# Kernel optimization log

Measured on AMD Instinct MI355X. Metric: run time of the kernel, lower is better.

The kernel has to match this reference:

```python
import jax, jax.numpy as jnp
from jax import lax
import numpy as np

N_FEATURES, HIDDEN, LATENT = 51, 64, 24
BATCH, SEQ = 2048, 100


def _lstm_params(key, in_dim, hid):
    k = 1.0 / np.sqrt(hid)
    ks = jax.random.split(key, 4)
    u = lambda kk, shape: jax.random.uniform(kk, shape, jnp.float32, -k, k)
    return (u(ks[0], (4 * hid, in_dim)),  # W_ih, torch gate order i,f,g,o
            u(ks[1], (4 * hid, hid)),     # W_hh
            u(ks[2], (4 * hid,)),         # b_ih
            u(ks[3], (4 * hid,)))         # b_hh


def lstm(x, w_ih, w_hh, b_ih, b_hh):
    """Batch-first single-layer LSTM matching torch.nn.LSTM (zero init state).
    x: [B,T,I] -> (outputs [B,T,H], final hidden [B,H])."""
    B = x.shape[0]
    H = w_hh.shape[1]
    # Precompute the input contribution for all timesteps in one GEMM.
    xg = jnp.einsum('bti,gi->btg', x, w_ih) + b_ih + b_hh  # [B,T,4H]

    def step(carry, xt):
        h, c = carry
        g = xt + h @ w_hh.T                       # [B,4H]
        i, f, gg, o = jnp.split(g, 4, axis=-1)    # torch order i,f,g,o
        i = jax.nn.sigmoid(i)
        f = jax.nn.sigmoid(f)
        gg = jnp.tanh(gg)
        o = jax.nn.sigmoid(o)
        c = f * c + i * gg
        h = o * jnp.tanh(c)
        return (h, c), h

    init = (jnp.zeros((B, H), x.dtype), jnp.zeros((B, H), x.dtype))
    (h_n, _), ys = lax.scan(step, init, jnp.swapaxes(xg, 0, 1))
    return jnp.swapaxes(ys, 0, 1), h_n


def setup_inputs() -> dict:
    key = jax.random.key(0)
    ks = jax.random.split(key, 6)
    x = jax.random.normal(ks[0], (BATCH, SEQ, N_FEATURES), jnp.float32)
    e1 = _lstm_params(ks[1], N_FEATURES, HIDDEN)
    e2 = _lstm_params(ks[2], HIDDEN, LATENT)
    d1 = _lstm_params(ks[3], LATENT, HIDDEN)
    d2 = _lstm_params(ks[4], HIDDEN, HIDDEN)
    kw, kb = jax.random.split(ks[5])
    kk = 1.0 / np.sqrt(HIDDEN)
    w_out = jax.random.uniform(kw, (N_FEATURES, HIDDEN), jnp.float32, -kk, kk)
    b_out = jax.random.uniform(kb, (N_FEATURES,), jnp.float32, -kk, kk)
    return {
        'x': x,
        'e1_wih': e1[0], 'e1_whh': e1[1], 'e1_bih': e1[2], 'e1_bhh': e1[3],
        'e2_wih': e2[0], 'e2_whh': e2[1], 'e2_bih': e2[2], 'e2_bhh': e2[3],
        'd1_wih': d1[0], 'd1_whh': d1[1], 'd1_bih': d1[2], 'd1_bhh': d1[3],
        'd2_wih': d2[0], 'd2_whh': d2[1], 'd2_bih': d2[2], 'd2_bhh': d2[3],
        'w_out': w_out, 'b_out': b_out,
    }


def reference(x,
              e1_wih, e1_whh, e1_bih, e1_bhh,
              e2_wih, e2_whh, e2_bih, e2_bhh,
              d1_wih, d1_whh, d1_bih, d1_bhh,
              d2_wih, d2_whh, d2_bih, d2_bhh,
              w_out, b_out):
    seq_len = x.shape[1]
    # Encode (dropout is identity at inference, p=0.1 train-only)
    out1, _ = lstm(x, e1_wih, e1_whh, e1_bih, e1_bhh)          # [B,T,hidden]
    _, z = lstm(out1, e2_wih, e2_whh, e2_bih, e2_bhh)          # hn -> [B,latent]
    # Decode: repeat latent across time
    rep = jnp.broadcast_to(z[:, None, :], (z.shape[0], seq_len, z.shape[1]))
    d_out1, _ = lstm(rep, d1_wih, d1_whh, d1_bih, d1_bhh)      # [B,T,hidden]
    d_out2, _ = lstm(d_out1, d2_wih, d2_whh, d2_bih, d2_bhh)   # [B,T,hidden]
    recon = jnp.einsum('bth,fh->btf', d_out2, w_out) + b_out   # [B,T,n_features]
    return recon
```

## Files before the change

kernel.cpp:

```cpp
#include <hip/hip_runtime.h>
#include <stdint.h>

typedef __attribute__((ext_vector_type(8))) __bf16 bf16x8;
typedef __attribute__((ext_vector_type(4))) float f32x4;
typedef __attribute__((ext_vector_type(4))) unsigned int uint4v;

#define DI __device__ __forceinline__
#define MFMA_(a,b,c) __builtin_amdgcn_mfma_f32_16x16x32_bf16(a,b,c,0,0,0)

static constexpr int B_ = 2048;
static constexpr int T_ = 100;

DI float bf2f(unsigned short u){
  unsigned int i = ((unsigned int)u) << 16;
  float f; __builtin_memcpy(&f, &i, 4); return f;
}
DI unsigned short f2bf(float f){
  unsigned int x; __builtin_memcpy(&x, &f, 4);
  unsigned int r = (x + 0x7fffu + ((x >> 16) & 1u)) >> 16;
  return (unsigned short)r;
}
DI unsigned int pk2bf(float a, float b){
  unsigned int r;
  asm("v_cvt_pk_bf16_f32 %0, %1, %2" : "=v"(r) : "v"(a), "v"(b));
  return r;
}
DI float rcp_(float x){ return __builtin_amdgcn_rcpf(x); }
DI float sig_(float x){ return rcp_(1.0f + __expf(-x)); }
DI float tanh_(float x){ return 1.0f - 2.0f * rcp_(__expf(2.0f * x) + 1.0f); }

template<int KS>
DI f32x4 dot1(const bf16x8* a, const bf16x8* b, f32x4 acc)
{
  #pragma unroll
  for (int s = 0; s < KS; ++s)
    acc = MFMA_(a[s], b[s], acc);
  return acc;
}

DI void pw(const f32x4 (&acc)[4], float (&cc)[4], float (&hv)[4],
           unsigned short (&hH)[4])
{
  #pragma unroll
  for (int r = 0; r < 4; ++r){
    float iv = sig_(acc[0][r]);
    float fv = sig_(acc[1][r]);
    float gv = tanh_(acc[2][r]);
    float ov = sig_(acc[3][r]);
    cc[r] = fv * cc[r] + iv * gv;
    hv[r] = ov * tanh_(cc[r]);
  }
  unsigned int u01 = pk2bf(hv[0], hv[1]);
  unsigned int u23 = pk2bf(hv[2], hv[3]);
  hH[0] = (unsigned short)u01; hH[1] = (unsigned short)(u01 >> 16);
  hH[2] = (unsigned short)u23; hH[3] = (unsigned short)(u23 >> 16);
}

__global__ __launch_bounds__(256) void prep_frags(
    const float* __restrict__ e1_wih, const float* __restrict__ e1_whh,
    const float* __restrict__ e2_wih, const float* __restrict__ e2_whh,
    const float* __restrict__ d1_whh,
    const float* __restrict__ d2_wih, const float* __restrict__ d2_whh,
    const float* __restrict__ w_out,
    unsigned short* __restrict__ dst)
{
  int fid = blockIdx.x * 256 + threadIdx.x;
  if (fid >= 12288) return;
  int layer, local, KS;
  if (fid < 4096)      { layer = 0; local = fid;         KS = 4; }
  else if (fid < 5632) { layer = 1; local = fid - 4096;  KS = 3; }
  else if (fid < 7680) { layer = 2; local = fid - 5632;  KS = 2; }
  else if (fid < 11776){ layer = 3; local = fid - 7680;  KS = 4; }
  else                 { layer = 4; local = fid - 11776; KS = 2; }
  int lane = local & 63;
  int ns = local >> 6;
  int s = ns % KS, n = ns / KS;
  int col = 16 * n + (lane & 15);
  int kb = 32 * s + 8 * (lane >> 4);
  union { unsigned short u[8]; uint4v v; } pk;
  #pragma unroll
  for (int e = 0; e < 8; ++e){
    int k = kb + e;
    float w = 0.0f;
    if (layer == 0){
      if (k < 51) w = e1_wih[col * 51 + k];
      else if (k >= 64) w = e1_whh[col * 64 + (k - 64)];
    } else if (layer == 1){
      int q = col >> 5, jj = col & 31;
      if (jj < 24){
        int r = q * 24 + jj;
        if (k < 64) w = e2_wih[r * 64 + k];
        else if (k < 88) w = e2_whh[r * 24 + (k - 64)];
      }
    } else if (layer == 2){
      w = d1_whh[col * 64 + k];
    } else if (layer == 3){
      if (k < 64) w = d2_wih[col * 64 + k];
      else w = d2_whh[col * 64 + (k - 64)];
    } else {
      if (col < 51) w = w_out[col * 64 + k];
    }
    pk.u[e] = f2bf(w);
  }
  *(uint4v*)(dst + (size_t)fid * 8) = pk.v;
}

__global__ __launch_bounds__(256) void gx_k(
    const float* __restrict__ z, const float* __restrict__ d1_wih,
    const float* __restrict__ bih, const float* __restrict__ bhh,
    float* __restrict__ gx)
{
  int s = blockIdx.x, col = threadIdx.x;
  float acc = bih[col] + bhh[col];
  #pragma unroll
  for (int k = 0; k < 24; ++k)
    acc += z[s * 24 + k] * d1_wih[col * 24 + k];
  gx[s * 256 + col] = acc;
}

__global__ __launch_bounds__(512, 1) void fused_enc(
    const float* xseq,
    const unsigned short* __restrict__ bf1u,
    const unsigned short* __restrict__ bf2u,
    const float* __restrict__ e1_bih, const float* __restrict__ e1_bhh,
    const float* __restrict__ e2_bih, const float* __restrict__ e2_bhh,
    float* __restrict__ zout)
{
  constexpr int SA1 = 136;
  constexpr int SB2 = 40;
  __shared__ __align__(16) unsigned short A1H[2][16 * SA1];
  __shared__ __align__(16) unsigned short A2B[2][16 * SB2];

  const int tid = threadIdx.x, wid = tid >> 6, lane = tid & 63;
  const int l15 = lane & 15, l4 = lane >> 4;
  const size_t s0 = (size_t)blockIdx.x * 16;
  const bool isE1 = (wid < 4);
  const bool isE2 = (wid == 4 || wid == 5);
  const bool isXW = (wid >= 6);
  const int jj1 = 16 * wid + l15;
  const int jj2 = 16 * (wid - 4) + l15;
  const int xt = tid - 384;

  const bf16x8* f1 = (const bf16x8*)bf1u;
  const bf16x8* f2 = (const bf16x8*)bf2u;
  bf16x8 b1H[16];
  f32x4 init1[4];
  if (isE1){
    #pragma unroll
    for (int g = 0; g < 4; ++g){
      #pragma unroll
      for (int s = 0; s < 4; ++s)
        b1H[g * 4 + s] = f1[(size_t)(((wid + 4 * g) * 4 + s) * 64 + lane)];
      float b = e1_bih[g * 64 + jj1] + e1_bhh[g * 64 + jj1];
      init1[g] = (f32x4){b, b, b, b};
    }
  }
  bf16x8 b2H[12];
  f32x4 init2[4];
  if (isE2){
    #pragma unroll
    for (int g = 0; g < 4; ++g){
      #pragma unroll
      for (int s = 0; s < 3; ++s)
        b2H[g * 3 + s] = f2[(size_t)((((wid - 4) + 2 * g) * 3 + s) * 64 + lane)];
      float b2 = (jj2 < 24) ? (e2_bih[g * 24 + jj2] + e2_bhh[g * 24 + jj2]) : 0.0f;
      init2[g] = (f32x4){b2, b2, b2, b2};
    }
  }

  for (int i = tid; i < 16 * SA1; i += 512){ A1H[0][i] = 0; A1H[1][i] = 0; }
  for (int i = tid; i < 16 * SB2; i += 512){ A2B[0][i] = 0; A2B[1][i] = 0; }
  __syncthreads();
  #pragma unroll
  for (int it = 0; it < 2; ++it){
    int idx = tid + it * 512, row = idx >> 6, k = idx & 63;
    float v = (k < 51) ? xseq[((s0 + row) * T_ + 0) * 51 + k] : 0.0f;
    A1H[0][row * SA1 + k] = f2bf(v);
  }
  __syncthreads();

  float xsA[8], xsB[8];
  if (isXW){
    #pragma unroll
    for (int it = 0; it < 8; ++it){
      int idx = xt + it * 128, row = idx >> 6, k = idx & 63;
      xsA[it] = (k < 51) ? xseq[((s0 + row) * T_ + 1) * 51 + k] : 0.0f;
      xsB[it] = (k < 51) ? xseq[((s0 + row) * T_ + 2) * 51 + k] : 0.0f;
    }
  }
  float cc1[4] = {0.f,0.f,0.f,0.f}, cc2[4] = {0.f,0.f,0.f,0.f};

#define ENC_STEP(TCUR, BSEL, XW)                                               \
  {                                                                            \
    const int t = (TCUR);                                                      \
    if (isE1 && t < T_){                                        \
      bf16x8 a1H[4];                                                           \
      _Pragma("unroll")                                                        \
      for (int s = 0; s < 4; ++s)                                              \
        a1H[s] = *(const bf16x8*)&A1H[BSEL][l15 * SA1 + 32 * s + 8 * l4];      \
      f32x4 acc[4];                                                            \
      _Pragma("unroll")                                                        \
      for (int g = 0; g < 4; ++g)                                              \
        acc[g] = dot1<4>(a1H, &b1H[g * 4], init1[g]);                          \
      float hv[4]; unsigned short hH[4];                                       \
      pw(acc, cc1, hv, hH);                                                    \
      _Pragma("unroll")                                                        \
      for (int r = 0; r < 4; ++r)                                              \
        A1H[BSEL ^ 1][(4 * l4 + r) * SA1 + 64 + jj1] = hH[r];                  \
    }                                                                          \
    if (isE2 && t >= 1 && t <= T_){                  \
      bf16x8 af2[3];                                                           \
      af2[0] = *(const bf16x8*)&A1H[BSEL][l15 * SA1 + 64 + 8 * l4];            \
      af2[1] = *(const bf16x8*)&A1H[BSEL][l15 * SA1 + 96 + 8 * l4];            \
      af2[2] = *(const bf16x8*)&A2B[BSEL][l15 * SB2 + 8 * l4];                 \
      f32x4 acc[4];                                                            \
      _Pragma("unroll")                                                        \
      for (int g = 0; g < 4; ++g)                                              \
        acc[g] = dot1<3>(af2, &b2H[g * 3], init2[g]);                          \
      float hv[4]; unsigned short hH[4];                                       \
      pw(acc, cc2, hv, hH);                                                    \
      if (jj2 < 24){                                                           \
        _Pragma("unroll")                                                      \
        for (int r = 0; r < 4; ++r)                                            \
          A2B[BSEL ^ 1][(4 * l4 + r) * SB2 + jj2] = hH[r];                     \
        if (t == T_){                                                          \
          _Pragma("unroll")                                                    \
          for (int r = 0; r < 4; ++r)                                          \
            zout[(s0 + 4 * l4 + r) * 24 + jj2] = hv[r];                        \
        }                                                                      \
      }                                                                        \
    }                                                                          \
    if (isXW && t + 1 < T_){             \
      _Pragma("unroll")                                                        \
      for (int it = 0; it < 8; it += 2){                                       \
        int idx = xt + it * 128;                                               \
        int row0_ = idx >> 6, k0_ = idx & 63;                                  \
        int row1_ = (idx + 128) >> 6, k1_ = (idx + 128) & 63;                  \
        unsigned int u = pk2bf(XW[it], XW[it + 1]);                            \
        A1H[BSEL ^ 1][row0_ * SA1 + k0_] = (unsigned short)u;                  \
        A1H[BSEL ^ 1][row1_ * SA1 + k1_] = (unsigned short)(u >> 16);          \
      }                                                                        \
      if (t + 3 < T_){                                                         \
        _Pragma("unroll")                                                      \
        for (int it = 0; it < 8; ++it){                                        \
          int idx = xt + it * 128, row = idx >> 6, k = idx & 63;               \
          XW[it] = (k < 51) ? xseq[((s0 + row) * T_ + (t + 3)) * 51 + k] : 0.0f; \
        }                                                                      \
      }                                                                        \
    }                                                                          \
    asm volatile("s_waitcnt lgkmcnt(0)\n\ts_barrier" ::: "memory");            \
  }

  #pragma unroll 1
  for (int tt = 0; tt < 102; tt += 2){
    ENC_STEP(tt,     0, xsA)
    ENC_STEP(tt + 1, 1, xsB)
  }
#undef ENC_STEP
}

__global__ __launch_bounds__(512, 1) void fused_dec(
    const float* __restrict__ gxin,
    const unsigned short* __restrict__ bf3u,
    const unsigned short* __restrict__ bf4u,
    const unsigned short* __restrict__ bfpu,
    const float* __restrict__ d2_bih, const float* __restrict__ d2_bhh,
    const float* __restrict__ b_out,
    float* out)
{
  constexpr int SA4 = 136;
  __shared__ __align__(16) unsigned short A4H[2][16 * SA4];

  const int tid = threadIdx.x, wid = tid >> 6, lane = tid & 63;
  const int l15 = lane & 15, l4 = lane >> 4;
  const size_t s0 = (size_t)blockIdx.x * 16;
  const bool isD1 = (wid < 4);
  const int jj3 = 16 * wid + l15;
  const int jj4 = 16 * (wid - 4) + l15;

  const bf16x8* f3 = (const bf16x8*)bf3u;
  const bf16x8* f4 = (const bf16x8*)bf4u;
  const bf16x8* fp = (const bf16x8*)bfpu;
  bf16x8 b3H[8], bpH[2];
  f32x4 init3[4], biasP;
  if (isD1){
    #pragma unroll
    for (int g = 0; g < 4; ++g){
      #pragma unroll
      for (int s = 0; s < 2; ++s)
        b3H[g * 2 + s] = f3[(size_t)(((wid + 4 * g) * 2 + s) * 64 + lane)];
      #pragma unroll
      for (int r = 0; r < 4; ++r)
        init3[g][r] = gxin[(s0 + 4 * l4 + r) * 256 + jj3 + 64 * g];
    }
    #pragma unroll
    for (int s = 0; s < 2; ++s)
      bpH[s] = fp[(size_t)((wid * 2 + s) * 64 + lane)];
    float bp = (jj3 < 51) ? b_out[jj3] : 0.0f;
    biasP = (f32x4){bp, bp, bp, bp};
  }
  bf16x8 b4H[16];
  f32x4 init4[4];
  if (!isD1){
    #pragma unroll
    for (int g = 0; g < 4; ++g){
      #pragma unroll
      for (int s = 0; s < 4; ++s)
        b4H[g * 4 + s] = f4[(size_t)((((wid - 4) + 4 * g) * 4 + s) * 64 + lane)];
      float b = d2_bih[g * 64 + jj4] + d2_bhh[g * 64 + jj4];
      init4[g] = (f32x4){b, b, b, b};
    }
  }

  for (int i = tid; i < 16 * SA4; i += 512){ A4H[0][i] = 0; A4H[1][i] = 0; }
  __syncthreads();

  float cc3[4] = {0.f,0.f,0.f,0.f}, cc4[4] = {0.f,0.f,0.f,0.f};

#define DEC_STEP(TCUR, BSEL)                                                   \
  {                                                                            \
    const int t = (TCUR);                                                      \
    bf16x8 a4[4];                                                              \
    _Pragma("unroll")                                                          \
    for (int s = 0; s < 4; ++s)                                                \
      a4[s] = *(const bf16x8*)&A4H[BSEL][l15 * SA4 + 32 * s + 8 * l4];         \
    if (isD1){                                                                 \
      if (t < T_){                     \
        f32x4 acc[4];                                                          \
        _Pragma("unroll")                                                      \
        for (int g = 0; g < 4; ++g)                                            \
          acc[g] = dot1<2>(a4, &b3H[g * 2], init3[g]);                         \
        float hv[4]; unsigned short hH[4];                                     \
        pw(acc, cc3, hv, hH);                                                  \
        _Pragma("unroll")                                                      \
        for (int r = 0; r < 4; ++r)                                            \
          A4H[BSEL ^ 1][(4 * l4 + r) * SA4 + jj3] = hH[r];                     \
      }                                                                        \
      if (t >= 2){                          \
        f32x4 pr = dot1<2>(&a4[2], bpH, biasP);                                \
        if (jj3 < 51){                                                         \
          _Pragma("unroll")                                                    \
          for (int r = 0; r < 4; ++r)                                          \
            out[((s0 + 4 * l4 + r) * T_ + (t - 2)) * 51 + jj3] = pr[r];        \
        }                                                                      \
      }                                                                        \
    } else {                                                                   \
      if (t >= 1 && t <= T_){                        \
        f32x4 acc[4];                                                          \
        _Pragma("unroll")                                                      \
        for (int g = 0; g < 4; ++g)                                            \
          acc[g] = dot1<4>(a4, &b4H[g * 4], init4[g]);                         \
        float hv[4]; unsigned short hH[4];                                     \
        pw(acc, cc4, hv, hH);                                                  \
        _Pragma("unroll")                                                      \
        for (int r = 0; r < 4; ++r)                                            \
          A4H[BSEL ^ 1][(4 * l4 + r) * SA4 + 64 + jj4] = hH[r];                \
      }                                                                        \
    }                                                                          \
    asm volatile("s_waitcnt lgkmcnt(0)\n\ts_barrier" ::: "memory");            \
  }

  #pragma unroll 1
  for (int tt = 0; tt < 102; tt += 2){
    DEC_STEP(tt,     0)
    DEC_STEP(tt + 1, 1)
  }
#undef DEC_STEP
}

extern "C" void kernel_launch(void* const* d_in, const int* in_sizes, int n_in,
                              void* d_out, int out_size, void* d_ws, size_t ws_size,
                              hipStream_t stream)
{
  (void)in_sizes; (void)n_in; (void)out_size; (void)ws_size;
  const float* x      = (const float*)d_in[0];
  const float* e1_wih = (const float*)d_in[1];
  const float* e1_whh = (const float*)d_in[2];
  const float* e1_bih = (const float*)d_in[3];
  const float* e1_bhh = (const float*)d_in[4];
  const float* e2_wih = (const float*)d_in[5];
  const float* e2_whh = (const float*)d_in[6];
  const float* e2_bih = (const float*)d_in[7];
  const float* e2_bhh = (const float*)d_in[8];
  const float* d1_wih = (const float*)d_in[9];
  const float* d1_whh = (const float*)d_in[10];
  const float* d1_bih = (const float*)d_in[11];
  const float* d1_bhh = (const float*)d_in[12];
  const float* d2_wih = (const float*)d_in[13];
  const float* d2_whh = (const float*)d_in[14];
  const float* d2_bih = (const float*)d_in[15];
  const float* d2_bhh = (const float*)d_in[16];
  const float* w_out  = (const float*)d_in[17];
  const float* b_out  = (const float*)d_in[18];

  char* ws = (char*)d_ws;
  unsigned short* bfrag = (unsigned short*)ws;
  const size_t OF_L2 = 4096 * 8, OF_L3 = 5632 * 8, OF_L4 = 7680 * 8, OF_PR = 11776 * 8;
  float* zbuf  = (float*)(ws + 196608);
  float* gxbuf = (float*)(ws + 196608 + 196608);

  prep_frags<<<48, 256, 0, stream>>>(e1_wih, e1_whh, e2_wih, e2_whh,
                                     d1_whh, d2_wih, d2_whh, w_out, bfrag);
  fused_enc<<<128, 512, 0, stream>>>(
      x, bfrag, bfrag + OF_L2, e1_bih, e1_bhh, e2_bih, e2_bhh, zbuf);
  gx_k<<<2048, 256, 0, stream>>>(zbuf, d1_wih, d1_bih, d1_bhh, gxbuf);
  fused_dec<<<128, 512, 0, stream>>>(
      gxbuf, bfrag + OF_L3, bfrag + OF_L4, bfrag + OF_PR,
      d2_bih, d2_bhh, b_out, (float*)d_out);
}
```

Baseline: 172.6 us.

## Fuse encoder, latent projection and decoder into one persistent kernel

Merges the encoder kernel, the small gx projection kernel and the decoder kernel into a single kernel. The latent z stays in shared memory and the d1 input projection is computed in registers, so the z and gx buffers no longer go through global memory. The time loops are peeled into prologue, steady-state and epilogue steps, which removes per-step bounds checks and lets shared-memory loads be issued before the MFMA work. This saves two kernel launches and a global round trip, at the cost of higher register pressure in one large kernel.

```diff
diff --git a/kernel.cpp b/kernel.cpp
--- a/kernel.cpp
+++ b/kernel.cpp
@@ -105,99 +105,97 @@
   *(uint4v*)(dst + (size_t)fid * 8) = pk.v;
 }
 
-__global__ __launch_bounds__(256) void gx_k(
-    const float* __restrict__ z, const float* __restrict__ d1_wih,
-    const float* __restrict__ bih, const float* __restrict__ bhh,
-    float* __restrict__ gx)
-{
-  int s = blockIdx.x, col = threadIdx.x;
-  float acc = bih[col] + bhh[col];
-  #pragma unroll
-  for (int k = 0; k < 24; ++k)
-    acc += z[s * 24 + k] * d1_wih[col * 24 + k];
-  gx[s * 256 + col] = acc;
-}
-
-__global__ __launch_bounds__(512, 1) void fused_enc(
+__global__ __launch_bounds__(512, 1) void fused_all(
     const float* xseq,
-    const unsigned short* __restrict__ bf1u,
-    const unsigned short* __restrict__ bf2u,
+    const unsigned short* __restrict__ bfr,
     const float* __restrict__ e1_bih, const float* __restrict__ e1_bhh,
     const float* __restrict__ e2_bih, const float* __restrict__ e2_bhh,
-    float* __restrict__ zout)
+    const float* __restrict__ d1_wih, const float* __restrict__ d1_bih,
+    const float* __restrict__ d1_bhh,
+    const float* __restrict__ d2_bih, const float* __restrict__ d2_bhh,
+    const float* __restrict__ b_out,
+    float* out)
 {
-  constexpr int SA1 = 136;
+  constexpr int SA = 136;
   constexpr int SB2 = 40;
-  __shared__ __align__(16) unsigned short A1H[2][16 * SA1];
+  constexpr size_t OF_L2 = 4096, OF_L3 = 5632, OF_L4 = 7680, OF_PR = 11776;
+  __shared__ __align__(16) unsigned short AST[2][16 * SA];
   __shared__ __align__(16) unsigned short A2B[2][16 * SB2];
+  __shared__ float zS[16][24];
 
   const int tid = threadIdx.x, wid = tid >> 6, lane = tid & 63;
   const int l15 = lane & 15, l4 = lane >> 4;
   const size_t s0 = (size_t)blockIdx.x * 16;
-  const bool isE1 = (wid < 4);
-  const bool isE2 = (wid == 4 || wid == 5);
-  const bool isXW = (wid >= 6);
-  const int jj1 = 16 * wid + l15;
-  const int jj2 = 16 * (wid - 4) + l15;
-  const int xt = tid - 384;
-
-  const bf16x8* f1 = (const bf16x8*)bf1u;
-  const bf16x8* f2 = (const bf16x8*)bf2u;
-  bf16x8 b1H[16];
-  f32x4 init1[4];
-  if (isE1){
+  const bf16x8* fr = (const bf16x8*)bfr;
+
+  {
+    const bool isE1 = (wid < 4);
+    const bool isE2 = (wid == 4 || wid == 5);
+    const bool isXW = (wid >= 6);
+    const int jj1 = 16 * wid + l15;
+    const int jj2 = 16 * (wid - 4) + l15;
+    const int xt = tid - 384;
+
+    bf16x8 b1H[16]; f32x4 init1[4];
+    if (isE1){
+      #pragma unroll
+      for (int g = 0; g < 4; ++g){
+        #pragma unroll
+        for (int s = 0; s < 4; ++s)
+          b1H[g * 4 + s] = fr[(size_t)(((wid + 4 * g) * 4 + s) * 64 + lane)];
+        float b = e1_bih[g * 64 + jj1] + e1_bhh[g * 64 + jj1];
+        init1[g] = (f32x4){b, b, b, b};
+      }
+    }
+    bf16x8 b2H[12]; f32x4 init2[4];
+    if (isE2){
+      #pragma unroll
+      for (int g = 0; g < 4; ++g){
+        #pragma unroll
+        for (int s = 0; s < 3; ++s)
+          b2H[g * 3 + s] = fr[OF_L2 + (size_t)((((wid - 4) + 2 * g) * 3 + s) * 64 + lane)];
+        float b2 = (jj2 < 24) ? (e2_bih[g * 24 + jj2] + e2_bhh[g * 24 + jj2]) : 0.0f;
+        init2[g] = (f32x4){b2, b2, b2, b2};
+      }
+    }
+
+    for (int i = tid; i < 16 * SA; i += 512){ AST[0][i] = 0; AST[1][i] = 0; }
+    for (int i = tid; i < 16 * SB2; i += 512){ A2B[0][i] = 0; A2B[1][i] = 0; }
+    __syncthreads();
     #pragma unroll
-    for (int g = 0; g < 4; ++g){
-      #pragma unroll
-      for (int s = 0; s < 4; ++s)
-        b1H[g * 4 + s] = f1[(size_t)(((wid + 4 * g) * 4 + s) * 64 + lane)];
-      float b = e1_bih[g * 64 + jj1] + e1_bhh[g * 64 + jj1];
-      init1[g] = (f32x4){b, b, b, b};
-    }
-  }
-  bf16x8 b2H[12];
-  f32x4 init2[4];
-  if (isE2){
-    #pragma unroll
-    for (int g = 0; g < 4; ++g){
-      #pragma unroll
-      for (int s = 0; s < 3; ++s)
-        b2H[g * 3 + s] = f2[(size_t)((((wid - 4) + 2 * g) * 3 + s) * 64 + lane)];
-      float b2 = (jj2 < 24) ? (e2_bih[g * 24 + jj2] + e2_bhh[g * 24 + jj2]) : 0.0f;
-      init2[g] = (f32x4){b2, b2, b2, b2};
-    }
-  }
-
-  for (int i = tid; i < 16 * SA1; i += 512){ A1H[0][i] = 0; A1H[1][i] = 0; }
-  for (int i = tid; i < 16 * SB2; i += 512){ A2B[0][i] = 0; A2B[1][i] = 0; }
-  __syncthreads();
-  #pragma unroll
-  for (int it = 0; it < 2; ++it){
-    int idx = tid + it * 512, row = idx >> 6, k = idx & 63;
-    float v = (k < 51) ? xseq[((s0 + row) * T_ + 0) * 51 + k] : 0.0f;
-    A1H[0][row * SA1 + k] = f2bf(v);
-  }
-  __syncthreads();
-
-  float xsA[8], xsB[8];
-  if (isXW){
-    #pragma unroll
-    for (int it = 0; it < 8; ++it){
-      int idx = xt + it * 128, row = idx >> 6, k = idx & 63;
-      xsA[it] = (k < 51) ? xseq[((s0 + row) * T_ + 1) * 51 + k] : 0.0f;
-      xsB[it] = (k < 51) ? xseq[((s0 + row) * T_ + 2) * 51 + k] : 0.0f;
-    }
-  }
-  float cc1[4] = {0.f,0.f,0.f,0.f}, cc2[4] = {0.f,0.f,0.f,0.f};
-
-#define ENC_STEP(TCUR, BSEL, XW)                                               \
+    for (int it = 0; it < 2; ++it){
+      int idx = tid + it * 512, row = idx >> 6, k = idx & 63;
+      float v = (k < 51) ? xseq[((s0 + row) * T_ + 0) * 51 + k] : 0.0f;
+      AST[0][row * SA + k] = f2bf(v);
+    }
+    __syncthreads();
+
+    float xsA[8], xsB[8];
+    if (isXW){
+      #pragma unroll
+      for (int it = 0; it < 8; ++it){
+        int idx = xt + it * 128, row = idx >> 6, k = idx & 63;
+        xsA[it] = (k < 51) ? xseq[((s0 + row) * T_ + 1) * 51 + k] : 0.0f;
+        xsB[it] = (k < 51) ? xseq[((s0 + row) * T_ + 2) * 51 + k] : 0.0f;
+      }
+    }
+    float cc1[4] = {0.f,0.f,0.f,0.f}, cc2[4] = {0.f,0.f,0.f,0.f};
+
+#define E_STEP(TT, BS, XW, D1, D2, DZ)                                         \
   {                                                                            \
-    const int t = (TCUR);                                                      \
-    if (isE1 && t < T_){                                        \
-      bf16x8 a1H[4];                                                           \
+    const int t = (TT);                                                        \
+    bf16x8 a1H[4]; bf16x8 af2[3];                                              \
+    if ((D1) && isE1){                                                         \
       _Pragma("unroll")                                                        \
       for (int s = 0; s < 4; ++s)                                              \
-        a1H[s] = *(const bf16x8*)&A1H[BSEL][l15 * SA1 + 32 * s + 8 * l4];      \
+        a1H[s] = *(const bf16x8*)&AST[BS][l15 * SA + 32 * s + 8 * l4];         \
+    }                                                                          \
+    if ((D2) && isE2){                                                         \
+      af2[0] = *(const bf16x8*)&AST[BS][l15 * SA + 64 + 8 * l4];               \
+      af2[1] = *(const bf16x8*)&AST[BS][l15 * SA + 96 + 8 * l4];               \
+      af2[2] = *(const bf16x8*)&A2B[BS][l15 * SB2 + 8 * l4];                   \
+    }                                                                          \
+    if ((D1) && isE1){                                                         \
       f32x4 acc[4];                                                            \
       _Pragma("unroll")                                                        \
       for (int g = 0; g < 4; ++g)                                              \
@@ -206,39 +204,17 @@
       pw(acc, cc1, hv, hH);                                                    \
       _Pragma("unroll")                                                        \
       for (int r = 0; r < 4; ++r)                                              \
-        A1H[BSEL ^ 1][(4 * l4 + r) * SA1 + 64 + jj1] = hH[r];                  \
-    }                                                                          \
-    if (isE2 && t >= 1 && t <= T_){                  \
-      bf16x8 af2[3];                                                           \
-      af2[0] = *(const bf16x8*)&A1H[BSEL][l15 * SA1 + 64 + 8 * l4];            \
-      af2[1] = *(const bf16x8*)&A1H[BSEL][l15 * SA1 + 96 + 8 * l4];            \
-      af2[2] = *(const bf16x8*)&A2B[BSEL][l15 * SB2 + 8 * l4];                 \
-      f32x4 acc[4];                                                            \
-      _Pragma("unroll")                                                        \
-      for (int g = 0; g < 4; ++g)                                              \
-        acc[g] = dot1<3>(af2, &b2H[g * 3], init2[g]);                          \
-      float hv[4]; unsigned short hH[4];                                       \
-      pw(acc, cc2, hv, hH);                                                    \
-      if (jj2 < 24){                                                           \
-        _Pragma("unroll")                                                      \
-        for (int r = 0; r < 4; ++r)                                            \
-          A2B[BSEL ^ 1][(4 * l4 + r) * SB2 + jj2] = hH[r];                     \
-        if (t == T_){                                                          \
-          _Pragma("unroll")                                                    \
-          for (int r = 0; r < 4; ++r)                                          \
-            zout[(s0 + 4 * l4 + r) * 24 + jj2] = hv[r];                        \
-        }                                                                      \
-      }                                                                        \
-    }                                                                          \
-    if (isXW && t + 1 < T_){             \
+        AST[BS ^ 1][(4 * l4 + r) * SA + 64 + jj1] = hH[r];                     \
+    }                                                                          \
+    if ((D1) && isXW && t + 1 < T_){                                           \
       _Pragma("unroll")                                                        \
       for (int it = 0; it < 8; it += 2){                                       \
         int idx = xt + it * 128;                                               \
         int row0_ = idx >> 6, k0_ = idx & 63;                                  \
         int row1_ = (idx + 128) >> 6, k1_ = (idx + 128) & 63;                  \
         unsigned int u = pk2bf(XW[it], XW[it + 1]);                            \
-        A1H[BSEL ^ 1][row0_ * SA1 + k0_] = (unsigned short)u;                  \
-        A1H[BSEL ^ 1][row1_ * SA1 + k1_] = (unsigned short)(u >> 16);          \
+        AST[BS ^ 1][row0_ * SA + k0_] = (unsigned short)u;                     \
+        AST[BS ^ 1][row1_ * SA + k1_] = (unsigned short)(u >> 16);             \
       }                                                                        \
       if (t + 3 < T_){                                                         \
         _Pragma("unroll")                                                      \
@@ -248,124 +224,154 @@
         }                                                                      \
       }                                                                        \
     }                                                                          \
+    if ((D2) && isE2){                                                         \
+      f32x4 acc[4];                                                            \
+      _Pragma("unroll")                                                        \
+      for (int g = 0; g < 4; ++g)                                              \
+        acc[g] = dot1<3>(af2, &b2H[g * 3], init2[g]);                          \
+      float hv[4]; unsigned short hH[4];                                       \
+      pw(acc, cc2, hv, hH);                                                    \
+      if (jj2 < 24){                                                           \
+        if (DZ){                                                               \
+          _Pragma("unroll")                                                    \
+          for (int r = 0; r < 4; ++r)                                          \
+            zS[4 * l4 + r][jj2] = hv[r];                                       \
+        } else {                                                               \
+          _Pragma("unroll")                                                    \
+          for (int r = 0; r < 4; ++r)                                          \
+            A2B[BS ^ 1][(4 * l4 + r) * SB2 + jj2] = hH[r];                     \
+        }                                                                      \
+      }                                                                        \
+    }                                                                          \
     asm volatile("s_waitcnt lgkmcnt(0)\n\ts_barrier" ::: "memory");            \
   }
 
-  #pragma unroll 1
-  for (int tt = 0; tt < 102; tt += 2){
-    ENC_STEP(tt,     0, xsA)
-    ENC_STEP(tt + 1, 1, xsB)
-  }
-#undef ENC_STEP
-}
-
-__global__ __launch_bounds__(512, 1) void fused_dec(
-    const float* __restrict__ gxin,
-    const unsigned short* __restrict__ bf3u,
-    const unsigned short* __restrict__ bf4u,
-    const unsigned short* __restrict__ bfpu,
-    const float* __restrict__ d2_bih, const float* __restrict__ d2_bhh,
-    const float* __restrict__ b_out,
-    float* out)
-{
-  constexpr int SA4 = 136;
-  __shared__ __align__(16) unsigned short A4H[2][16 * SA4];
-
-  const int tid = threadIdx.x, wid = tid >> 6, lane = tid & 63;
-  const int l15 = lane & 15, l4 = lane >> 4;
-  const size_t s0 = (size_t)blockIdx.x * 16;
-  const bool isD1 = (wid < 4);
-  const int jj3 = 16 * wid + l15;
-  const int jj4 = 16 * (wid - 4) + l15;
-
-  const bf16x8* f3 = (const bf16x8*)bf3u;
-  const bf16x8* f4 = (const bf16x8*)bf4u;
-  const bf16x8* fp = (const bf16x8*)bfpu;
-  bf16x8 b3H[8], bpH[2];
-  f32x4 init3[4], biasP;
-  if (isD1){
-    #pragma unroll
-    for (int g = 0; g < 4; ++g){
+    E_STEP(0, 0, xsA, 1, 0, 0)
+    #pragma unroll 1
+    for (int tt = 1; tt < 99; tt += 2){
+      E_STEP(tt,     1, xsB, 1, 1, 0)
+      E_STEP(tt + 1, 0, xsA, 1, 1, 0)
+    }
+    E_STEP(99, 1, xsB, 1, 1, 0)
+    E_STEP(100, 0, xsA, 0, 1, 1)
+#undef E_STEP
+  }
+
+  {
+    const bool isD1 = (wid < 4);
+    const int jj3 = 16 * wid + l15;
+    const int jj4 = 16 * (wid - 4) + l15;
+
+    bf16x8 b3H[8], bpH[2], b4H[16];
+    f32x4 init3[4], init4[4], biasP;
+    if (isD1){
+      #pragma unroll
+      for (int g = 0; g < 4; ++g){
+        #pragma unroll
+        for (int s = 0; s < 2; ++s)
+          b3H[g * 2 + s] = fr[OF_L3 + (size_t)(((wid + 4 * g) * 2 + s) * 64 + lane)];
+        float b = d1_bih[g * 64 + jj3] + d1_bhh[g * 64 + jj3];
+        init3[g] = (f32x4){b, b, b, b};
+      }
       #pragma unroll
       for (int s = 0; s < 2; ++s)
-        b3H[g * 2 + s] = f3[(size_t)(((wid + 4 * g) * 2 + s) * 64 + lane)];
-      #pragma unroll
-      for (int r = 0; r < 4; ++r)
-        init3[g][r] = gxin[(s0 + 4 * l4 + r) * 256 + jj3 + 64 * g];
-    }
-    #pragma unroll
-    for (int s = 0; s < 2; ++s)
-      bpH[s] = fp[(size_t)((wid * 2 + s) * 64 + lane)];
-    float bp = (jj3 < 51) ? b_out[jj3] : 0.0f;
-    biasP = (f32x4){bp, bp, bp, bp};
-  }
-  bf16x8 b4H[16];
-  f32x4 init4[4];
-  if (!isD1){
-    #pragma unroll
-    for (int g = 0; g < 4; ++g){
-      #pragma unroll
-      for (int s = 0; s < 4; ++s)
-        b4H[g * 4 + s] = f4[(size_t)((((wid - 4) + 4 * g) * 4 + s) * 64 + lane)];
-      float b = d2_bih[g * 64 + jj4] + d2_bhh[g * 64 + jj4];
-      init4[g] = (f32x4){b, b, b, b};
-    }
-  }
-
-  for (int i = tid; i < 16 * SA4; i += 512){ A4H[0][i] = 0; A4H[1][i] = 0; }
-  __syncthreads();
-
-  float cc3[4] = {0.f,0.f,0.f,0.f}, cc4[4] = {0.f,0.f,0.f,0.f};
-
-#define DEC_STEP(TCUR, BSEL)                                                   \
+        bpH[s] = fr[OF_PR + (size_t)((wid * 2 + s) * 64 + lane)];
+      float bp = (jj3 < 51) ? b_out[jj3] : 0.0f;
+      biasP = (f32x4){bp, bp, bp, bp};
+    } else {
+      #pragma unroll
+      for (int g = 0; g < 4; ++g){
+        #pragma unroll
+        for (int s = 0; s < 4; ++s)
+          b4H[g * 4 + s] = fr[OF_L4 + (size_t)((((wid - 4) + 4 * g) * 4 + s) * 64 + lane)];
+        float b = d2_bih[g * 64 + jj4] + d2_bhh[g * 64 + jj4];
+        init4[g] = (f32x4){b, b, b, b};
+      }
+    }
+
+    for (int i = tid; i < 16 * SA; i += 512){ AST[0][i] = 0; AST[1][i] = 0; }
+
+    if (isD1){
+      #pragma unroll 1
+      for (int k = 0; k < 24; ++k){
+        float z0 = zS[4 * l4 + 0][k], z1 = zS[4 * l4 + 1][k];
+        float z2 = zS[4 * l4 + 2][k], z3 = zS[4 * l4 + 3][k];
+        #pragma unroll
+        for (int g = 0; g < 4; ++g){
+          float w = d1_wih[(jj3 + 64 * g) * 24 + k];
+          init3[g][0] += z0 * w; init3[g][1] += z1 * w;
+          init3[g][2] += z2 * w; init3[g][3] += z3 * w;
+        }
+      }
+    }
+    __syncthreads();
+
+    float cc3[4] = {0.f,0.f,0.f,0.f}, cc4[4] = {0.f,0.f,0.f,0.f};
+    constexpr int R51 = T_ * 51;
+    float* op = out + (s0 + 4 * l4) * (size_t)R51 + jj3;
+
+#define D_STEP(BS, D1F, D2F, PRF)                                              \
   {                                                                            \
-    const int t = (TCUR);                                                      \
     bf16x8 a4[4];                                                              \
-    _Pragma("unroll")                                                          \
-    for (int s = 0; s < 4; ++s)                                                \
-      a4[s] = *(const bf16x8*)&A4H[BSEL][l15 * SA4 + 32 * s + 8 * l4];         \
     if (isD1){                                                                 \
-      if (t < T_){                     \
-        f32x4 acc[4];                                                          \
-        _Pragma("unroll")                                                      \
-        for (int g = 0; g < 4; ++g)                                            \
-          acc[g] = dot1<2>(a4, &b3H[g * 2], init3[g]);                         \
-        float hv[4]; unsigned short hH[4];                                     \
-        pw(acc, cc3, hv, hH);                                                  \
+      if (D1F){                                                                \
+        a4[0] = *(const bf16x8*)&AST[BS][l15 * SA + 8 * l4];                   \
+        a4[1] = *(const bf16x8*)&AST[BS][l15 * SA + 32 + 8 * l4];              \
+      }                                                                        \
+      if (PRF){                                                                \
+        a4[2] = *(const bf16x8*)&AST[BS][l15 * SA + 64 + 8 * l4];              \
+        a4[3] = *(const bf16x8*)&AST[BS][l15 * SA + 96 + 8 * l4];              \
+      }                                                                        \
+    } else if (D2F){                                                           \
+      _Pragma("unroll")                                                        \
+      for (int s = 0; s < 4; ++s)                                              \
+        a4[s] = *(const bf16x8*)&AST[BS][l15 * SA + 32 * s + 8 * l4];          \
+    }                                                                          \
+    if (isD1 && (D1F)){                                                        \
+      f32x4 acc[4];                                                            \
+      _Pragma("unroll")                                                        \
+      for (int g = 0; g < 4; ++g)                                              \
+        acc[g] = dot1<2>(a4, &b3H[g * 2], init3[g]);                           \
+      float hv[4]; unsigned short hH[4];                                       \
+      pw(acc, cc3, hv, hH);                                                    \
+      _Pragma("unroll")                                                        \
+      for (int r = 0; r < 4; ++r)                                              \
+        AST[BS ^ 1][(4 * l4 + r) * SA + jj3] = hH[r];                          \
+    }                                                                          \
+    if (!isD1 && (D2F)){                                                       \
+      f32x4 acc[4];                                                            \
+      _Pragma("unroll")                                                        \
+      for (int g = 0; g < 4; ++g)                                              \
+        acc[g] = dot1<4>(a4, &b4H[g * 4], init4[g]);                           \
+      float hv[4]; unsigned short hH[4];                                       \
+      pw(acc, cc4, hv, hH);                                                    \
+      _Pragma("unroll")                                                        \
+      for (int r = 0; r < 4; ++r)                                              \
+        AST[BS ^ 1][(4 * l4 + r) * SA + 64 + jj4] = hH[r];                     \
+    }                                                                          \
+    if (isD1 && (PRF)){                                                        \
+      f32x4 pr = dot1<2>(&a4[2], bpH, biasP);                                  \
+      if (jj3 < 51){                                                           \
         _Pragma("unroll")                                                      \
         for (int r = 0; r < 4; ++r)                                            \
-          A4H[BSEL ^ 1][(4 * l4 + r) * SA4 + jj3] = hH[r];                     \
-      }                                                                        \
-      if (t >= 2){                          \
-        f32x4 pr = dot1<2>(&a4[2], bpH, biasP);                                \
-        if (jj3 < 51){                                                         \
-          _Pragma("unroll")                                                    \
-          for (int r = 0; r < 4; ++r)                                          \
-            out[((s0 + 4 * l4 + r) * T_ + (t - 2)) * 51 + jj3] = pr[r];        \
-        }                                                                      \
-      }                                                                        \
-    } else {                                                                   \
-      if (t >= 1 && t <= T_){                        \
-        f32x4 acc[4];                                                          \
-        _Pragma("unroll")                                                      \
-        for (int g = 0; g < 4; ++g)                                            \
-          acc[g] = dot1<4>(a4, &b4H[g * 4], init4[g]);                         \
-        float hv[4]; unsigned short hH[4];                                     \
-        pw(acc, cc4, hv, hH);                                                  \
-        _Pragma("unroll")                                                      \
-        for (int r = 0; r < 4; ++r)                                            \
-          A4H[BSEL ^ 1][(4 * l4 + r) * SA4 + 64 + jj4] = hH[r];                \
-      }                                                                        \
+          op[r * R51] = pr[r];                                                 \
+      }                                                                        \
+      op += 51;                                                                \
     }                                                                          \
     asm volatile("s_waitcnt lgkmcnt(0)\n\ts_barrier" ::: "memory");            \
   }
 
-  #pragma unroll 1
-  for (int tt = 0; tt < 102; tt += 2){
-    DEC_STEP(tt,     0)
-    DEC_STEP(tt + 1, 1)
-  }
-#undef DEC_STEP
+    D_STEP(0, 1, 0, 0)
+    D_STEP(1, 1, 1, 0)
+    #pragma unroll 1
+    for (int tt = 2; tt < 100; tt += 2){
+      D_STEP(0, 1, 1, 1)
+      D_STEP(1, 1, 1, 1)
+    }
+    D_STEP(0, 0, 1, 1)
+    D_STEP(1, 0, 0, 1)
+#undef D_STEP
+  }
 }
 
 extern "C" void kernel_launch(void* const* d_in, const int* in_sizes, int n_in,
@@ -393,18 +399,14 @@
   const float* w_out  = (const float*)d_in[17];
   const float* b_out  = (const float*)d_in[18];
 
-  char* ws = (char*)d_ws;
-  unsigned short* bfrag = (unsigned short*)ws;
-  const size_t OF_L2 = 4096 * 8, OF_L3 = 5632 * 8, OF_L4 = 7680 * 8, OF_PR = 11776 * 8;
-  float* zbuf  = (float*)(ws + 196608);
-  float* gxbuf = (float*)(ws + 196608 + 196608);
+  unsigned short* bfrag = (unsigned short*)d_ws;
 
   prep_frags<<<48, 256, 0, stream>>>(e1_wih, e1_whh, e2_wih, e2_whh,
                                      d1_whh, d2_wih, d2_whh, w_out, bfrag);
-  fused_enc<<<128, 512, 0, stream>>>(
-      x, bfrag, bfrag + OF_L2, e1_bih, e1_bhh, e2_bih, e2_bhh, zbuf);
-  gx_k<<<2048, 256, 0, stream>>>(zbuf, d1_wih, d1_bih, d1_bhh, gxbuf);
-  fused_dec<<<128, 512, 0, stream>>>(
-      gxbuf, bfrag + OF_L3, bfrag + OF_L4, bfrag + OF_PR,
-      d2_bih, d2_bhh, b_out, (float*)d_out);
-}
+  fused_all<<<128, 512, 0, stream>>>(
+      x, bfrag,
+      e1_bih, e1_bhh, e2_bih, e2_bhh,
+      d1_wih, d1_bih, d1_bhh,
+      d2_bih, d2_bhh, b_out,
+      (float*)d_out);
+}
```

After: 227.4 us. 1.32x slower.
